# Kernel tuning notes

Hardware: AMD Instinct MI355X
Metric: run time of the kernel (lower is better)

Reference implementation:

```python
import jax, jax.numpy as jnp
import numpy as np

EPS = 1e-5

def _layernorm(x, w, b):
    mu = jnp.mean(x, axis=-1, keepdims=True)
    var = jnp.mean(jnp.square(x - mu), axis=-1, keepdims=True)
    return (x - mu) * jax.lax.rsqrt(var + EPS) * w + b

def setup_inputs() -> dict:
    key = jax.random.key(0)
    ks = jax.random.split(key, 8)
    B, N, D = 1, 512, 128
    x = jax.random.normal(ks[0], (B, N, N, D), dtype=jnp.float32)
    mask = jnp.ones((B, N, N), dtype=jnp.float32)
    # learned params (torch nn.Linear stores weight as (out, in))
    p_in_w = jax.random.normal(ks[1], (2 * D, D), dtype=jnp.float32) * (1.0 / np.sqrt(D))
    g_in_w = jax.random.normal(ks[2], (2 * D, D), dtype=jnp.float32) * 0.02
    p_out_w = jax.random.normal(ks[3], (D, D), dtype=jnp.float32) * 0.02
    g_out_w = jax.random.normal(ks[4], (D, D), dtype=jnp.float32) * 0.02
    norm_in_w = jnp.ones((D,), dtype=jnp.float32)
    norm_in_b = jnp.zeros((D,), dtype=jnp.float32)
    norm_out_w = jnp.ones((D,), dtype=jnp.float32)
    norm_out_b = jnp.zeros((D,), dtype=jnp.float32)
    return {"x": x, "mask": mask, "norm_in_w": norm_in_w, "norm_in_b": norm_in_b,
            "p_in_w": p_in_w, "g_in_w": g_in_w, "norm_out_w": norm_out_w,
            "norm_out_b": norm_out_b, "p_out_w": p_out_w, "g_out_w": g_out_w}

def reference(x, mask, norm_in_w, norm_in_b, p_in_w, g_in_w, norm_out_w, norm_out_b, p_out_w, g_out_w):
    # x: (B,N,N,D), mask: (B,N,N)
    x_ln = _layernorm(x, norm_in_w, norm_in_b)          # (B,N,N,D)
    x_in = x_ln
    # gated dual projection to 2D channels, then mask
    h = jnp.einsum('bijd,ed->bije', x_ln, p_in_w) * jax.nn.sigmoid(
        jnp.einsum('bijd,ed->bije', x_ln, g_in_w))      # (B,N,N,2D)
    h = h * mask[..., None]
    D = x.shape[-1]
    a, b = h[..., :D], h[..., D:]                        # (B,N,N,D) each
    # triangular 'outgoing' contraction over k
    t = jnp.einsum('bikd,bjkd->bijd', a, b)              # (B,N,N,D)
    out = jnp.einsum('bijd,ed->bije', _layernorm(t, norm_out_w, norm_out_b), p_out_w) \
        * jax.nn.sigmoid(jnp.einsum('bijd,ed->bije', x_in, g_out_w))
    return out
```

## Files before the change

kernel.cpp:

```cpp
#include <hip/hip_runtime.h>
#include <stdint.h>

#define NSEQ 512
#define DDIM 128
#define NROWS (NSEQ * NSEQ)
#define PMASK (NROWS - 1)
#define ROT(idx, d) (((idx) + (d) * 128) & PMASK)

typedef __bf16 bf16x8 __attribute__((ext_vector_type(8)));
typedef __bf16 bf16x2v __attribute__((ext_vector_type(2)));
typedef unsigned short u16;
typedef u16 ushort8 __attribute__((ext_vector_type(8)));
typedef float f32x4 __attribute__((ext_vector_type(4)));
typedef uint32_t u32x4 __attribute__((ext_vector_type(4)));
typedef uint32_t u32x2 __attribute__((ext_vector_type(2)));

__device__ __forceinline__ u16 cvt1(float f) {
  return __builtin_bit_cast(u16, (__bf16)f);
}
__device__ __forceinline__ uint32_t pk2(float a, float b) {
  bf16x2v v = {(__bf16)a, (__bf16)b};
  return __builtin_bit_cast(uint32_t, v);
}
__device__ __forceinline__ float bf2f(u16 u) {
  uint32_t x = ((uint32_t)u) << 16;
  return __builtin_bit_cast(float, x);
}
__device__ __forceinline__ f32x4 mfma_bf16(ushort8 a, ushort8 b, f32x4 c) {
  return __builtin_amdgcn_mfma_f32_16x16x32_bf16(
      __builtin_bit_cast(bf16x8, a), __builtin_bit_cast(bf16x8, b), c, 0, 0, 0);
}
__device__ __forceinline__ float sigmoidf_(float x) {
  return __builtin_amdgcn_rcpf(1.0f + __expf(-x));
}

#define ROR16(v, n)                                                            \
  __builtin_bit_cast(float, __builtin_amdgcn_update_dpp(                       \
      __builtin_bit_cast(int, (v)), __builtin_bit_cast(int, (v)),              \
      0x120 + (n), 0xF, 0xF, false))

#define GLOAD16(gp, lp)                                                        \
  __builtin_amdgcn_global_load_lds(                                            \
      (const __attribute__((address_space(1))) void*)(gp),                     \
      (__attribute__((address_space(3))) void*)(lp), 16, 0, 0)

__global__ __launch_bounds__(256) void k0_prep(
    const float* __restrict__ p_in_w, const float* __restrict__ g_in_w,
    const float* __restrict__ p_out_w, const float* __restrict__ g_out_w,
    const float* __restrict__ now, const float* __restrict__ nob,
    u16* __restrict__ Wb, u16* __restrict__ Pb, u16* __restrict__ Gb,
    float* __restrict__ S12) {
  const int b = blockIdx.x, t = threadIdx.x;
#pragma unroll
  for (int k = 0; k < 2; ++k) {
    const int idx = b * 512 + k * 256 + t;
    const float v = (idx < 32768) ? p_in_w[idx] : g_in_w[idx - 32768];
    Wb[idx] = cvt1(v);
  }
  if (t < 128) {
    const int idx = b * 128 + t;
    const int d = idx & 127;
    Pb[idx] = cvt1(p_out_w[idx] * now[d]);
    Gb[idx] = cvt1(g_out_w[idx]);
  }
  const int w = t >> 6, lane = t & 63;
  if (w >= 2) {
    const float* wv = (w == 2) ? now : nob;
    float p = p_out_w[b * 128 + lane] * wv[lane] +
              p_out_w[b * 128 + 64 + lane] * wv[64 + lane];
#pragma unroll
    for (int m = 1; m < 64; m <<= 1) p += __shfl_xor(p, m);
    if (lane == 0) S12[2 * b + (w - 2)] = p;
  }
}

__global__ __launch_bounds__(256, 6) void k1_ln_proj(
    const float* __restrict__ x, const float* __restrict__ mask,
    const float* __restrict__ niw, const float* __restrict__ nib,
    const u16* __restrict__ Wb, const u16* __restrict__ Gb,
    u16* __restrict__ At, u16* __restrict__ Bt, u16* __restrict__ gArg) {
  __shared__ __align__(16) u16 xln[64 * 128];
  __shared__ __align__(16) u16 stage[64 * 64];
  const int tid = threadIdx.x;
  const int lane = tid & 63;
  const int w = tid >> 6;
  const int bid = blockIdx.x;
  const int rb = (bid >> 5) * 8 + (bid & 7);
  const int cg = (bid >> 3) & 3;
  const int r0 = rb * 64;
  const int g = lane >> 4, c = lane & 15;

  f32x4 v0[4], v1[4];
#pragma unroll
  for (int it = 0; it < 4; ++it) {
    const int rl = w * 16 + it * 4 + g;
    const float* xr = x + (size_t)(r0 + rl) * DDIM + c * 8;
    v0[it] = *(const f32x4*)xr;
    v1[it] = *(const f32x4*)(xr + 4);
  }
  const f32x4 w0 = *(const f32x4*)(niw + c * 8);
  const f32x4 w1 = *(const f32x4*)(niw + c * 8 + 4);
  const f32x4 b0 = *(const f32x4*)(nib + c * 8);
  const f32x4 b1 = *(const f32x4*)(nib + c * 8 + 4);
#pragma unroll
  for (int it = 0; it < 4; ++it) {
    const int rl = w * 16 + it * 4 + g;
    float s = v0[it][0] + v0[it][1] + v0[it][2] + v0[it][3] +
              v1[it][0] + v1[it][1] + v1[it][2] + v1[it][3];
    float ss = v0[it][0] * v0[it][0] + v0[it][1] * v0[it][1] +
               v0[it][2] * v0[it][2] + v0[it][3] * v0[it][3] +
               v1[it][0] * v1[it][0] + v1[it][1] * v1[it][1] +
               v1[it][2] * v1[it][2] + v1[it][3] * v1[it][3];
    { float t1 = ROR16(s, 1); s += t1; t1 = ROR16(ss, 1); ss += t1; }
    { float t1 = ROR16(s, 2); s += t1; t1 = ROR16(ss, 2); ss += t1; }
    { float t1 = ROR16(s, 4); s += t1; t1 = ROR16(ss, 4); ss += t1; }
    { float t1 = ROR16(s, 8); s += t1; t1 = ROR16(ss, 8); ss += t1; }
    const float mu = s * (1.0f / 128.0f);
    const float rs = rsqrtf(ss * (1.0f / 128.0f) - mu * mu + 1e-5f);
    float f0 = (v0[it][0] - mu) * rs * w0[0] + b0[0];
    float f1 = (v0[it][1] - mu) * rs * w0[1] + b0[1];
    float f2 = (v0[it][2] - mu) * rs * w0[2] + b0[2];
    float f3 = (v0[it][3] - mu) * rs * w0[3] + b0[3];
    float f4 = (v1[it][0] - mu) * rs * w1[0] + b1[0];
    float f5 = (v1[it][1] - mu) * rs * w1[1] + b1[1];
    float f6 = (v1[it][2] - mu) * rs * w1[2] + b1[2];
    float f7 = (v1[it][3] - mu) * rs * w1[3] + b1[3];
    u32x4 ov{pk2(f0, f1), pk2(f2, f3), pk2(f4, f5), pk2(f6, f7)};
    const int byteoff = rl * 256 + ((c ^ (rl & 7)) << 4);
    *(u32x4*)((char*)xln + byteoff) = ov;
  }
  __syncthreads();

  const int lr = lane & 15, lq = lane >> 4;
  const int eP = cg * 64 + w * 16;
  f32x4 accP[4], accG[4];
#pragma unroll
  for (int m = 0; m < 4; ++m) {
    accP[m] = f32x4{0.f, 0.f, 0.f, 0.f};
    accG[m] = f32x4{0.f, 0.f, 0.f, 0.f};
  }

#pragma unroll
  for (int ks = 0; ks < 4; ++ks) {
    const int kblk = ks * 4 + lq;
    ushort8 af[4];
#pragma unroll
    for (int m = 0; m < 4; ++m) {
      const int row = m * 16 + lr;
      af[m] = *(const ushort8*)((const char*)xln + row * 256 +
                                ((kblk ^ (row & 7)) << 4));
    }
    const int e = eP + lr;
    const int dd = ks * 32 + lq * 8;
    const ushort8 bP = *(const ushort8*)(Wb + e * 128 + dd);
    const ushort8 bG = *(const ushort8*)(Wb + (256 + e) * 128 + dd);
#pragma unroll
    for (int m = 0; m < 4; ++m) {
      accP[m] = mfma_bf16(af[m], bP, accP[m]);
      accG[m] = mfma_bf16(af[m], bG, accG[m]);
    }
  }

  const int dloc = w * 16 + lr;
#pragma unroll
  for (int m = 0; m < 4; ++m) {
    const int rloc = m * 16 + lq * 4;
    const f32x4 mv = *(const f32x4*)(mask + r0 + rloc);
    const float o0 = accP[m][0] * sigmoidf_(accG[m][0]) * mv[0];
    const float o1 = accP[m][1] * sigmoidf_(accG[m][1]) * mv[1];
    const float o2 = accP[m][2] * sigmoidf_(accG[m][2]) * mv[2];
    const float o3 = accP[m][3] * sigmoidf_(accG[m][3]) * mv[3];
    u32x2 pk;
    pk[0] = pk2(o0, o1);
    pk[1] = pk2(o2, o3);
    const int gsw = (m * 4 + lq) ^ (dloc & 15);
    *(u32x2*)((char*)stage + dloc * 128 + (gsw << 3)) = pk;
  }
  __syncthreads();

  {
    u16* dstbase = (cg >= 2) ? Bt : At;
    const int colbase = (cg & 1) * 64;
    const int R = tid >> 1;
    const int dl = R >> 1, seg = R & 1;
    const int dcol = colbase + dl;
#pragma unroll
    for (int rr = 0; rr < 2; ++rr) {
      const int il = (tid & 1) * 2 + rr;
      const int g0 = seg * 8 + il * 2;
      const u32x2 lo =
          *(const u32x2*)((const char*)stage + dl * 128 + ((g0 ^ (dl & 15)) << 3));
      const u32x2 hi = *(const u32x2*)((const char*)stage + dl * 128 +
                                       (((g0 + 1) ^ (dl & 15)) << 3));
      u32x4 outv{lo[0], lo[1], hi[0], hi[1]};
      const int ridx = ROT(r0 + seg * 32 + il * 8, dcol);
      *(u32x4*)(dstbase + (size_t)dcol * NROWS + ridx) = outv;
    }
  }

  if (cg < 2) {
    f32x4 accO[4];
#pragma unroll
    for (int m = 0; m < 4; ++m) accO[m] = f32x4{0.f, 0.f, 0.f, 0.f};
    const int eg = cg * 64 + w * 16 + lr;
#pragma unroll
    for (int ks = 0; ks < 4; ++ks) {
      const int kblk = ks * 4 + lq;
      const ushort8 bO = *(const ushort8*)(Gb + eg * 128 + ks * 32 + lq * 8);
#pragma unroll
      for (int m = 0; m < 4; ++m) {
        const int row = m * 16 + lr;
        const ushort8 af2 = *(const ushort8*)((const char*)xln + row * 256 +
                                              ((kblk ^ (row & 7)) << 4));
        accO[m] = mfma_bf16(af2, bO, accO[m]);
      }
    }
    __syncthreads();
    u16* stage2 = stage;
    const int e_loc = w * 16 + lr;
    const int gsl = e_loc >> 2;
    const int esub = (e_loc & 3) * 2;
#pragma unroll
    for (int m = 0; m < 4; ++m) {
#pragma unroll
      for (int reg = 0; reg < 4; ++reg) {
        const int rl2 = m * 16 + lq * 4 + reg;
        *(u16*)((char*)stage2 + rl2 * 128 + ((gsl ^ (rl2 & 7)) << 3) + esub) =
            cvt1(accO[m][reg]);
      }
    }
    __syncthreads();
#pragma unroll
    for (int p = 0; p < 2; ++p) {
      const int r = p * 32 + (tid >> 3);
      const int il8 = tid & 7;
      const char* base = (const char*)stage2 + r * 128;
      const u32x2 a = *(const u32x2*)(base + (((il8 * 2) ^ (r & 7)) << 3));
      const u32x2 b = *(const u32x2*)(base + (((il8 * 2 + 1) ^ (r & 7)) << 3));
      u32x4 ov{a[0], a[1], b[0], b[1]};
      *(u32x4*)(gArg + (size_t)(r0 + r) * DDIM + cg * 64 + il8 * 8) = ov;
    }
  }
}

__global__ __launch_bounds__(256) void k2_tri(const u16* __restrict__ At,
                                              const u16* __restrict__ Bt,
                                              u16* __restrict__ Ct) {
  __shared__ __align__(16) u16 lds[2 * 16384];
  const int tid = threadIdx.x;
  const int bid = blockIdx.x;
  const int lb = (bid & 7) * 256 + (bid >> 3);
  const int d = lb >> 4;
  const int tile = lb & 15;
  const int i0 = (tile >> 2) * 128, j0 = (tile & 3) * 128;
  const u16* Ad = At + (size_t)d * NROWS;
  const u16* Bd = Bt + (size_t)d * NROWS;
  const int lane = tid & 63, wid = tid >> 6;
  const int wr = wid >> 1, wc = wid & 1;
  const int lr = lane & 15, lq = lane >> 4;

  f32x4 acc[4][4];
#pragma unroll
  for (int m = 0; m < 4; ++m)
#pragma unroll
    for (int n = 0; n < 4; ++n) acc[m][n] = f32x4{0.f, 0.f, 0.f, 0.f};

  auto stage = [&](int kt, int buf) {
    const int k0 = kt * 64;
#pragma unroll
    for (int q = 0; q < 4; ++q) {
      const int idx = q * 256 + tid;
      const int r = idx >> 3, bk = idx & 7;
      const int sbk = bk ^ (r & 7);
      GLOAD16(Ad + ROT((i0 + r) * NSEQ + k0 + sbk * 8, d),
              &lds[buf * 16384 + idx * 8]);
      GLOAD16(Bd + ROT((j0 + r) * NSEQ + k0 + sbk * 8, d),
              &lds[buf * 16384 + 8192 + idx * 8]);
    }
  };

  stage(0, 0);
  __syncthreads();
  for (int kt = 0; kt < 8; ++kt) {
    const int buf = kt & 1;
    if (kt < 7) stage(kt + 1, buf ^ 1);
    const u16* A_l = &lds[buf * 16384];
    const u16* B_l = &lds[buf * 16384 + 8192];
#pragma unroll
    for (int ks = 0; ks < 2; ++ks) {
      const int kblk = ks * 4 + lq;
      ushort8 af[4], bfr[4];
#pragma unroll
      for (int m = 0; m < 4; ++m) {
        const int row = wr * 64 + m * 16 + lr;
        af[m] = *(const ushort8*)((const char*)A_l + row * 128 +
                                  ((kblk ^ (row & 7)) << 4));
      }
#pragma unroll
      for (int n = 0; n < 4; ++n) {
        const int col = wc * 64 + n * 16 + lr;
        bfr[n] = *(const ushort8*)((const char*)B_l + col * 128 +
                                   ((kblk ^ (col & 7)) << 4));
      }
#pragma unroll
      for (int m = 0; m < 4; ++m)
#pragma unroll
        for (int n = 0; n < 4; ++n)
          acc[m][n] = mfma_bf16(af[m], bfr[n], acc[m][n]);
    }
    __syncthreads();
  }

  u16* Cd = Ct + (size_t)d * NROWS;
#pragma unroll
  for (int m = 0; m < 4; ++m) {
    const int i = i0 + wr * 64 + m * 16 + lq * 4;
#pragma unroll
    for (int n = 0; n < 4; ++n) {
      const int j = j0 + wc * 64 + n * 16 + lr;
#pragma unroll
      for (int reg = 0; reg < 4; ++reg)
        Cd[ROT((i + reg) * NSEQ + j, d)] = cvt1(acc[m][n][reg]);
    }
  }
}

__global__ __launch_bounds__(256, 4) void k3_out(
    const u16* __restrict__ Ct, const u16* __restrict__ gArg,
    const u16* __restrict__ Pb, const float* __restrict__ S12,
    float* __restrict__ out) {
  __shared__ __align__(16) u16 ldsT[128 * 128];
  __shared__ float ps[4 * 128], pss[4 * 128];
  __shared__ float prm[128 * 2];
  __shared__ float s12l[128 * 2];
  const int tid = threadIdx.x, lane = tid & 63, w = tid >> 6;
  const int c0 = blockIdx.x * 128;

  {
    const int row2 = lane * 2;
    float s0 = 0.f, ss0 = 0.f, s1 = 0.f, ss1 = 0.f;
#pragma unroll
    for (int db = 0; db < 4; ++db) {
      uint32_t pe[4], po[4];
#pragma unroll
      for (int j = 0; j < 8; ++j) {
        const int d = w * 32 + db * 8 + j;
        const uint32_t v = *(const uint32_t*)(Ct + (size_t)d * NROWS +
                                              ROT(c0 + row2, d));
        const u16 ue = (u16)v, uo = (u16)(v >> 16);
        const float fe = bf2f(ue), fo = bf2f(uo);
        s0 += fe; ss0 += fe * fe;
        s1 += fo; ss1 += fo * fo;
        if (j & 1) {
          pe[j >> 1] |= ((uint32_t)ue) << 16;
          po[j >> 1] |= ((uint32_t)uo) << 16;
        } else {
          pe[j >> 1] = ue;
          po[j >> 1] = uo;
        }
      }
      const int gr = w * 4 + db;
      *(u32x4*)((char*)ldsT + row2 * 256 + ((gr ^ (row2 & 7)) << 4)) =
          u32x4{pe[0], pe[1], pe[2], pe[3]};
      *(u32x4*)((char*)ldsT + (row2 + 1) * 256 + ((gr ^ ((row2 + 1) & 7)) << 4)) =
          u32x4{po[0], po[1], po[2], po[3]};
    }
    ps[w * 128 + row2] = s0;
    pss[w * 128 + row2] = ss0;
    ps[w * 128 + row2 + 1] = s1;
    pss[w * 128 + row2 + 1] = ss1;
  }
  if (tid < 128) ((u32x2*)s12l)[tid] = ((const u32x2*)S12)[tid];
  __syncthreads();
  if (tid < 128) {
    const float s = ps[tid] + ps[128 + tid] + ps[256 + tid] + ps[384 + tid];
    const float ss = pss[tid] + pss[128 + tid] + pss[256 + tid] + pss[384 + tid];
    const float mu = s * (1.f / 128.f);
    const float rs = rsqrtf(ss * (1.f / 128.f) - mu * mu + 1e-5f);
    prm[2 * tid] = rs;
    prm[2 * tid + 1] = -rs * mu;
  }

  const int lr = lane & 15, lq = lane >> 4;
  const int rowbase = w * 32;
  f32x4 aP[2][8];
#pragma unroll
  for (int m = 0; m < 2; ++m)
#pragma unroll
    for (int n = 0; n < 8; ++n) aP[m][n] = f32x4{0.f, 0.f, 0.f, 0.f};
#pragma unroll
  for (int ks = 0; ks < 4; ++ks) {
    const int kblk = ks * 4 + lq;
    ushort8 at2[2];
#pragma unroll
    for (int m = 0; m < 2; ++m) {
      const int row = rowbase + m * 16 + lr;
      at2[m] = *(const ushort8*)((const char*)ldsT + row * 256 +
                                 ((kblk ^ (row & 7)) << 4));
    }
    ushort8 bp[8];
#pragma unroll
    for (int n = 0; n < 8; ++n) {
      const int e = n * 16 + lr;
      bp[n] = *(const ushort8*)(Pb + e * 128 + ks * 32 + lq * 8);
    }
#pragma unroll
    for (int m = 0; m < 2; ++m)
#pragma unroll
      for (int n = 0; n < 8; ++n) aP[m][n] = mfma_bf16(at2[m], bp[n], aP[m][n]);
  }
  __syncthreads();

#pragma unroll
  for (int m = 0; m < 2; ++m) {
    const int crow = rowbase + m * 16 + lq * 4;
#pragma unroll
    for (int n = 0; n < 8; ++n) {
      const int e = n * 16 + lr;
      const float s1 = s12l[2 * e], s2v = s12l[2 * e + 1];
#pragma unroll
      for (int reg = 0; reg < 4; ++reg) {
        const float rs = prm[2 * (crow + reg)];
        const float t1 = prm[2 * (crow + reg) + 1];
        const float op = rs * aP[m][n][reg] + t1 * s1 + s2v;
        const size_t r = (size_t)(c0 + crow + reg);
        const float gt = sigmoidf_(bf2f(gArg[r * DDIM + e]));
        out[r * DDIM + e] = op * gt;
      }
    }
  }
}

extern "C" void kernel_launch(void* const* d_in, const int* in_sizes, int n_in,
                              void* d_out, int out_size, void* d_ws,
                              size_t ws_size, hipStream_t stream) {
  const float* x = (const float*)d_in[0];
  const float* mask = (const float*)d_in[1];
  const float* niw = (const float*)d_in[2];
  const float* nib = (const float*)d_in[3];
  const float* p_in_w = (const float*)d_in[4];
  const float* g_in_w = (const float*)d_in[5];
  const float* now = (const float*)d_in[6];
  const float* nob = (const float*)d_in[7];
  const float* p_out_w = (const float*)d_in[8];
  const float* g_out_w = (const float*)d_in[9];
  float* out = (float*)d_out;
  char* ws = (char*)d_ws;

  u16* At = (u16*)(ws);
  u16* Bt = (u16*)(ws + 67108864);
  u16* Ct = (u16*)(ws + 134217728);
  u16* gA = (u16*)(ws + 201326592);
  u16* Wb = (u16*)(ws + 268435456);
  u16* Pb = (u16*)(ws + 268566528);
  u16* Gb = (u16*)(ws + 268599296);
  float* S12 = (float*)(ws + 268632064);

  hipLaunchKernelGGL(k0_prep, dim3(128), dim3(256), 0, stream, p_in_w, g_in_w,
                     p_out_w, g_out_w, now, nob, Wb, Pb, Gb, S12);
  hipLaunchKernelGGL(k1_ln_proj, dim3(4 * NROWS / 64), dim3(256), 0, stream, x,
                     mask, niw, nib, Wb, Gb, At, Bt, gA);
  hipLaunchKernelGGL(k2_tri, dim3(128 * 16), dim3(256), 0, stream, At, Bt, Ct);
  hipLaunchKernelGGL(k3_out, dim3(NROWS / 128), dim3(256), 0, stream, Ct, gA,
                     Pb, S12, out);
}
```

Before: 322.3 us.

## Store A and B projections in a blocked k-tile layout shared by both kernels

Replaces the separate per-channel transposed A and B buffers, which used rotated row indexing, with a single blocked buffer indexed by k-tile, row and channel, with 64 contiguous k values per entry. The projection kernel now writes each staged tile as contiguous 128-byte rows instead of scattered per-channel strided stores. The contraction kernel reads 64-element k chunks for each row and channel from this layout. The aim is to make the projection kernel's global writes contiguous and drop the rotation arithmetic, at the cost of the contraction kernel's loads now striding across the channel dimension.

```diff
diff --git a/kernel.cpp b/kernel.cpp
--- a/kernel.cpp
+++ b/kernel.cpp
@@ -78,7 +78,7 @@
     const float* __restrict__ x, const float* __restrict__ mask,
     const float* __restrict__ niw, const float* __restrict__ nib,
     const u16* __restrict__ Wb, const u16* __restrict__ Gb,
-    u16* __restrict__ At, u16* __restrict__ Bt, u16* __restrict__ gArg) {
+    u16* __restrict__ AtB, u16* __restrict__ gArg) {
   __shared__ __align__(16) u16 xln[64 * 128];
   __shared__ __align__(16) u16 stage[64 * 64];
   const int tid = threadIdx.x;
@@ -179,22 +179,18 @@
   __syncthreads();
 
   {
-    u16* dstbase = (cg >= 2) ? Bt : At;
-    const int colbase = (cg & 1) * 64;
-    const int R = tid >> 1;
-    const int dl = R >> 1, seg = R & 1;
-    const int dcol = colbase + dl;
-#pragma unroll
-    for (int rr = 0; rr < 2; ++rr) {
-      const int il = (tid & 1) * 2 + rr;
-      const int g0 = seg * 8 + il * 2;
+    const int i_ = rb >> 3, kt = rb & 7;
+    u16* dst = AtB + (((size_t)kt * 512 + i_) * 256 + cg * 64) * 64;
+#pragma unroll
+    for (int q = 0; q < 2; ++q) {
+      const int e = q * 32 + (tid >> 3);
+      const int g0 = (tid & 7) * 2;
       const u32x2 lo =
-          *(const u32x2*)((const char*)stage + dl * 128 + ((g0 ^ (dl & 15)) << 3));
-      const u32x2 hi = *(const u32x2*)((const char*)stage + dl * 128 +
-                                       (((g0 + 1) ^ (dl & 15)) << 3));
+          *(const u32x2*)((const char*)stage + e * 128 + ((g0 ^ (e & 15)) << 3));
+      const u32x2 hi = *(const u32x2*)((const char*)stage + e * 128 +
+                                       (((g0 + 1) ^ (e & 15)) << 3));
       u32x4 outv{lo[0], lo[1], hi[0], hi[1]};
-      const int ridx = ROT(r0 + seg * 32 + il * 8, dcol);
-      *(u32x4*)(dstbase + (size_t)dcol * NROWS + ridx) = outv;
+      *(u32x4*)(dst + e * 64 + (tid & 7) * 8) = outv;
     }
   }
 
@@ -243,8 +239,7 @@
   }
 }
 
-__global__ __launch_bounds__(256) void k2_tri(const u16* __restrict__ At,
-                                              const u16* __restrict__ Bt,
+__global__ __launch_bounds__(256) void k2_tri(const u16* __restrict__ AtB,
                                               u16* __restrict__ Ct) {
   __shared__ __align__(16) u16 lds[2 * 16384];
   const int tid = threadIdx.x;
@@ -253,8 +248,6 @@
   const int d = lb >> 4;
   const int tile = lb & 15;
   const int i0 = (tile >> 2) * 128, j0 = (tile & 3) * 128;
-  const u16* Ad = At + (size_t)d * NROWS;
-  const u16* Bd = Bt + (size_t)d * NROWS;
   const int lane = tid & 63, wid = tid >> 6;
   const int wr = wid >> 1, wc = wid & 1;
   const int lr = lane & 15, lq = lane >> 4;
@@ -266,15 +259,14 @@
     for (int n = 0; n < 4; ++n) acc[m][n] = f32x4{0.f, 0.f, 0.f, 0.f};
 
   auto stage = [&](int kt, int buf) {
-    const int k0 = kt * 64;
 #pragma unroll
     for (int q = 0; q < 4; ++q) {
       const int idx = q * 256 + tid;
       const int r = idx >> 3, bk = idx & 7;
       const int sbk = bk ^ (r & 7);
-      GLOAD16(Ad + ROT((i0 + r) * NSEQ + k0 + sbk * 8, d),
+      GLOAD16(AtB + (((size_t)kt * 512 + i0 + r) * 256 + d) * 64 + sbk * 8,
               &lds[buf * 16384 + idx * 8]);
-      GLOAD16(Bd + ROT((j0 + r) * NSEQ + k0 + sbk * 8, d),
+      GLOAD16(AtB + (((size_t)kt * 512 + j0 + r) * 256 + 128 + d) * 64 + sbk * 8,
               &lds[buf * 16384 + 8192 + idx * 8]);
     }
   };
@@ -447,8 +439,7 @@
   float* out = (float*)d_out;
   char* ws = (char*)d_ws;
 
-  u16* At = (u16*)(ws);
-  u16* Bt = (u16*)(ws + 67108864);
+  u16* AtB = (u16*)(ws);
   u16* Ct = (u16*)(ws + 134217728);
   u16* gA = (u16*)(ws + 201326592);
   u16* Wb = (u16*)(ws + 268435456);
@@ -459,8 +450,8 @@
   hipLaunchKernelGGL(k0_prep, dim3(128), dim3(256), 0, stream, p_in_w, g_in_w,
                      p_out_w, g_out_w, now, nob, Wb, Pb, Gb, S12);
   hipLaunchKernelGGL(k1_ln_proj, dim3(4 * NROWS / 64), dim3(256), 0, stream, x,
-                     mask, niw, nib, Wb, Gb, At, Bt, gA);
-  hipLaunchKernelGGL(k2_tri, dim3(128 * 16), dim3(256), 0, stream, At, Bt, Ct);
+                     mask, niw, nib, Wb, Gb, AtB, gA);
+  hipLaunchKernelGGL(k2_tri, dim3(128 * 16), dim3(256), 0, stream, AtB, Ct);
   hipLaunchKernelGGL(k3_out, dim3(NROWS / 128), dim3(256), 0, stream, Ct, gA,
                      Pb, S12, out);
 }
```

Result: no change. 321.7 us (-0.2%).
